# Performance work log

Measured on AMD Instinct MI355X. Metric: run time of the kernel, lower is better.

## Reference

```python
import jax, jax.numpy as jnp
import numpy as np

B, T, E, H = 2, 1024, 1024, 16
D = E // H  # per-head dim = 64; softmax scale uses sqrt(D) per SelfAttentionHead.embedding_dim
SCALE = float(np.sqrt(D))


def setup_inputs() -> dict:
    key = jax.random.key(0)
    ks = jax.random.split(key, 10)
    s = 1.0 / np.sqrt(D)
    sf = 1.0 / np.sqrt(E)
    return {
        "x": jax.random.normal(ks[0], (B, T, E), dtype=jnp.float32),
        # per-head linear params, stacked over head index i: (H, D, D) / (H, D)
        "Wq": jax.random.uniform(ks[1], (H, D, D), minval=-s, maxval=s, dtype=jnp.float32),
        "bq": jax.random.uniform(ks[2], (H, D), minval=-s, maxval=s, dtype=jnp.float32),
        "Wk": jax.random.uniform(ks[3], (H, D, D), minval=-s, maxval=s, dtype=jnp.float32),
        "bk": jax.random.uniform(ks[4], (H, D), minval=-s, maxval=s, dtype=jnp.float32),
        "Wv": jax.random.uniform(ks[5], (H, D, D), minval=-s, maxval=s, dtype=jnp.float32),
        "bv": jax.random.uniform(ks[6], (H, D), minval=-s, maxval=s, dtype=jnp.float32),
        "Wf": jax.random.uniform(ks[7], (E, E), minval=-sf, maxval=sf, dtype=jnp.float32),
        "bf": jax.random.uniform(ks[8], (E,), minval=-sf, maxval=sf, dtype=jnp.float32),
    }


def reference(x, Wq, bq, Wk, bk, Wv, bv, Wf, bf):
    # (B, T, E) -> (B, H, T, D)
    xh = x.reshape(B, T, H, D).transpose(0, 2, 1, 3)
    # each head i applies its own D->D linears to the FULL (B,H,T,D) tensor
    # q/k/v: (B, H, T, I, D) where I indexes the head (param set)
    q = jnp.einsum('bhtd,ied->bhtie', xh, Wq) + bq
    k = jnp.einsum('bhtd,ied->bhtie', xh, Wk) + bk
    v = jnp.einsum('bhtd,ied->bhtie', xh, Wv) + bv
    # attention over the FEATURE dimension: scores are (B,H,I,D,D)
    scores = jnp.einsum('bhtip,bhtiq->bhipq', q, k) / SCALE
    w = jax.nn.softmax(scores, axis=-1)
    # (B,H,I,D,D) x (B,H,T,I,D) -> (B,H,T,I,D)
    o = jnp.einsum('bhipq,bhtiq->bhtip', w, v)
    # concat head outputs along last dim: (B,H,T,I*D) = (B,H,T,E)
    cat = o.reshape(B, H, T, E)
    # final Linear(E,E)
    return jnp.einsum('bhte,fe->bhtf', cat, Wf) + bf
```

## Files before the change

kernel.cpp:

```cpp
#include <hip/hip_runtime.h>

#define TT 1024
#define EE 1024

typedef __attribute__((ext_vector_type(8))) short short8;
typedef __attribute__((ext_vector_type(4))) float floatx4;
typedef __attribute__((ext_vector_type(4))) unsigned short ushort4v;
typedef __attribute__((ext_vector_type(8))) unsigned short ushort8v;

static __device__ __forceinline__ unsigned short f2bf(float f) {
  union { float f; unsigned int u; } v; v.f = f;
  unsigned int u = v.u;
  u += 0x7FFFu + ((u >> 16) & 1u);
  return (unsigned short)(u >> 16);
}
static __device__ __forceinline__ float bf2f(unsigned short u) {
  union { unsigned int i; float f; } v; v.i = ((unsigned int)u) << 16;
  return v.f;
}
static __device__ __forceinline__ void splitbf(float x, unsigned short& h,
                                               unsigned short& l) {
  h = f2bf(x);
  l = f2bf(x - bf2f(h));
}
static __device__ __forceinline__ unsigned short* lp(const unsigned short* t,
                                                     int row, int byte) {
  return (unsigned short*)((const char*)t + row * 128 + (byte ^ ((row & 7) << 4)));
}
static __device__ __forceinline__ short8 ldf(const unsigned short* t, int row,
                                             int byte) {
  return *(const short8*)((const char*)t + row * 128 + (byte ^ ((row & 7) << 4)));
}

__global__ __launch_bounds__(256) void kP(const float* __restrict__ x,
                                          const float* __restrict__ Wf,
                                          float* __restrict__ Sxx_part,
                                          float* __restrict__ sx_part,
                                          unsigned short* __restrict__ Wfbf,
                                          unsigned short* __restrict__ xbf) {
  const int bx = blockIdx.x;
  const int r = threadIdx.x;
  if (bx >= 256) {
    const int wb = bx - 256;
#pragma unroll
    for (int it = 0; it < 4; ++it) {
      int idx = wb * 4096 + it * 1024 + r * 4;
      float4 v = *reinterpret_cast<const float4*>(&Wf[idx]);
      ushort4v o;
      o[0] = f2bf(v.x); o[1] = f2bf(v.y); o[2] = f2bf(v.z); o[3] = f2bf(v.w);
      *reinterpret_cast<ushort4v*>(&Wfbf[idx]) = o;
    }
    return;
  }
  const int bh = bx >> 3, chunk = bx & 7;
  const int b = bh >> 4, h = bh & 15;
  const int t0 = chunk * 128;
  __shared__ float Xs[128 * 64];
  const float* xb = x + ((size_t)b * TT + t0) * EE + h * 64;
#pragma unroll
  for (int j = 0; j < 8; ++j) {
    int idx4 = j * 256 + r;
    int t = idx4 >> 4, c4 = idx4 & 15;
    *reinterpret_cast<float4*>(&Xs[t * 64 + c4 * 4]) =
        *reinterpret_cast<const float4*>(&xb[(size_t)t * EE + c4 * 4]);
  }
  __syncthreads();
#pragma unroll
  for (int j = 0; j < 4; ++j) {
    int idx8 = j * 256 + r;
    int t = idx8 >> 3, gch = idx8 & 7;
    ushort8v o;
#pragma unroll
    for (int e = 0; e < 8; ++e) o[e] = f2bf(Xs[t * 64 + gch * 8 + e]);
    *reinterpret_cast<ushort8v*>(&xbf[((size_t)bh * TT + t0 + t) * 64 + gch * 8]) = o;
  }
  const int p0 = (r >> 4) * 4, q0 = (r & 15) * 4;
  float acc[4][4] = {};
  for (int t = 0; t < 128; ++t) {
    float4 pv = *reinterpret_cast<const float4*>(&Xs[t * 64 + p0]);
    float4 qv = *reinterpret_cast<const float4*>(&Xs[t * 64 + q0]);
    float pa[4] = {pv.x, pv.y, pv.z, pv.w};
    float qa[4] = {qv.x, qv.y, qv.z, qv.w};
#pragma unroll
    for (int i = 0; i < 4; ++i)
#pragma unroll
      for (int j = 0; j < 4; ++j) acc[i][j] += pa[i] * qa[j];
  }
  float* Sb = Sxx_part + ((size_t)chunk * 32 + bh) * 4096;
#pragma unroll
  for (int i = 0; i < 4; ++i) {
    float4 v = make_float4(acc[i][0], acc[i][1], acc[i][2], acc[i][3]);
    *reinterpret_cast<float4*>(&Sb[(p0 + i) * 64 + q0]) = v;
  }
  if (r < 64) {
    float s = 0.f;
    for (int t = 0; t < 128; ++t) s += Xs[t * 64 + r];
    sx_part[(chunk * 32 + bh) * 64 + r] = s;
  }
}

__global__ __launch_bounds__(256) void kB1(const float* __restrict__ Sxx_part,
                                           const float* __restrict__ sx_part,
                                           const float* __restrict__ Wq,
                                           const float* __restrict__ bq,
                                           const float* __restrict__ Wk,
                                           const float* __restrict__ bk,
                                           const float* __restrict__ Wv,
                                           const float* __restrict__ bv,
                                           unsigned short* __restrict__ Mtbf) {
  const int blk = blockIdx.x;
  const int bh = blk >> 4, ih = blk & 15;
  const int r = threadIdx.x;
  const int w = r >> 6, l = r & 63;
  const int wm = w >> 1, wn = w & 1;
  const int lm = l & 15, lk = l >> 4;

  __shared__ unsigned short TSh[4096], TSl[4096];
  __shared__ unsigned short TWh[4096], TWl[4096];
  __shared__ unsigned short TAh[4096], TAl[4096];
  __shared__ float SC[64 * 68];
  __shared__ float svec[64], qsv[64], ksv[64], bqv[64], bkv[64], bvv[64];

#pragma unroll
  for (int it = 0; it < 4; ++it) {
    int idx = it * 1024 + r * 4;
    int row = idx >> 6, c0 = idx & 63;
    float4 vs = *(const float4*)&Sxx_part[(size_t)bh * 4096 + idx];
#pragma unroll
    for (int ch = 1; ch < 8; ++ch) {
      float4 tv = *(const float4*)&Sxx_part[((size_t)ch * 32 + bh) * 4096 + idx];
      vs.x += tv.x; vs.y += tv.y; vs.z += tv.z; vs.w += tv.w;
    }
    float4 vw = *(const float4*)&Wq[ih * 4096 + idx];
    float fs[4] = {vs.x, vs.y, vs.z, vs.w};
    float fw[4] = {vw.x, vw.y, vw.z, vw.w};
    ushort4v sh, sl, wh, wl;
#pragma unroll
    for (int j = 0; j < 4; ++j) {
      unsigned short th, tl;
      splitbf(fs[j], th, tl);
      sh[j] = th; sl[j] = tl;
      splitbf(fw[j], th, tl);
      wh[j] = th; wl[j] = tl;
    }
    *(ushort4v*)lp(TSh, row, c0 * 2) = sh;
    *(ushort4v*)lp(TSl, row, c0 * 2) = sl;
    *(ushort4v*)lp(TWh, row, c0 * 2) = wh;
    *(ushort4v*)lp(TWl, row, c0 * 2) = wl;
  }
  if (r < 64) {
    float s = 0.f;
#pragma unroll
    for (int ch = 0; ch < 8; ++ch) s += sx_part[(ch * 32 + bh) * 64 + r];
    svec[r] = s;
    bqv[r] = bq[ih * 64 + r];
    bkv[r] = bk[ih * 64 + r];
    bvv[r] = bv[ih * 64 + r];
  }
  __syncthreads();

  floatx4 a1[2][2] = {};
  {
    short8 Ah[2][2], Al[2][2], Bh[2][2], Bl[2][2];
#pragma unroll
    for (int mt = 0; mt < 2; ++mt)
#pragma unroll
      for (int ks = 0; ks < 2; ++ks) {
        Ah[mt][ks] = ldf(TWh, wm * 32 + mt * 16 + lm, ks * 64 + lk * 16);
        Al[mt][ks] = ldf(TWl, wm * 32 + mt * 16 + lm, ks * 64 + lk * 16);
        Bh[mt][ks] = ldf(TSh, wn * 32 + mt * 16 + lm, ks * 64 + lk * 16);
        Bl[mt][ks] = ldf(TSl, wn * 32 + mt * 16 + lm, ks * 64 + lk * 16);
      }
#pragma unroll
    for (int ks = 0; ks < 2; ++ks)
#pragma unroll
      for (int mt = 0; mt < 2; ++mt)
#pragma unroll
        for (int nt = 0; nt < 2; ++nt) {
          a1[mt][nt] = __builtin_amdgcn_mfma_f32_16x16x32_bf16(Ah[mt][ks], Bh[nt][ks], a1[mt][nt], 0, 0, 0);
          a1[mt][nt] = __builtin_amdgcn_mfma_f32_16x16x32_bf16(Ah[mt][ks], Bl[nt][ks], a1[mt][nt], 0, 0, 0);
          a1[mt][nt] = __builtin_amdgcn_mfma_f32_16x16x32_bf16(Al[mt][ks], Bh[nt][ks], a1[mt][nt], 0, 0, 0);
        }
  }
#pragma unroll
  for (int mt = 0; mt < 2; ++mt)
#pragma unroll
    for (int nt = 0; nt < 2; ++nt)
#pragma unroll
      for (int q = 0; q < 4; ++q) {
        int p = wm * 32 + mt * 16 + lk * 4 + q;
        int dd = wn * 32 + nt * 16 + lm;
        unsigned short h, lo2;
        splitbf(a1[mt][nt][q], h, lo2);
        *lp(TAh, p, dd * 2) = h;
        *lp(TAl, p, dd * 2) = lo2;
      }
  {
    int p = r >> 2, dc = (r & 3) * 16;
    float s = 0.f;
#pragma unroll
    for (int j = 0; j < 16; ++j) {
      int d = dc + j;
      s += (bf2f(*lp(TWh, p, d * 2)) + bf2f(*lp(TWl, p, d * 2))) * svec[d];
    }
    s += __shfl_xor(s, 1);
    s += __shfl_xor(s, 2);
    if ((r & 3) == 0) qsv[p] = s;
  }
  __syncthreads();

#pragma unroll
  for (int it = 0; it < 4; ++it) {
    int idx = it * 1024 + r * 4;
    int row = idx >> 6, c0 = idx & 63;
    float4 vw = *(const float4*)&Wk[ih * 4096 + idx];
    float fw[4] = {vw.x, vw.y, vw.z, vw.w};
    ushort4v wh, wl;
#pragma unroll
    for (int j = 0; j < 4; ++j) {
      unsigned short th, tl;
      splitbf(fw[j], th, tl);
      wh[j] = th; wl[j] = tl;
    }
    *(ushort4v*)lp(TWh, row, c0 * 2) = wh;
    *(ushort4v*)lp(TWl, row, c0 * 2) = wl;
    float4 vv = *(const float4*)&Wv[ih * 4096 + idx];
    int q = row, d0 = c0;
    *lp(TSh, d0 + 0, q * 2) = f2bf(vv.x);
    *lp(TSh, d0 + 1, q * 2) = f2bf(vv.y);
    *lp(TSh, d0 + 2, q * 2) = f2bf(vv.z);
    *lp(TSh, d0 + 3, q * 2) = f2bf(vv.w);
  }
  __syncthreads();
  {
    int p = r >> 2, dc = (r & 3) * 16;
    float s = 0.f;
#pragma unroll
    for (int j = 0; j < 16; ++j) {
      int d = dc + j;
      s += (bf2f(*lp(TWh, p, d * 2)) + bf2f(*lp(TWl, p, d * 2))) * svec[d];
    }
    s += __shfl_xor(s, 1);
    s += __shfl_xor(s, 2);
    if ((r & 3) == 0) ksv[p] = s;
  }
  floatx4 a2[2][2] = {};
  {
    short8 Ah[2][2], Al[2][2], Bh[2][2], Bl[2][2];
#pragma unroll
    for (int mt = 0; mt < 2; ++mt)
#pragma unroll
      for (int ks = 0; ks < 2; ++ks) {
        Ah[mt][ks] = ldf(TAh, wm * 32 + mt * 16 + lm, ks * 64 + lk * 16);
        Al[mt][ks] = ldf(TAl, wm * 32 + mt * 16 + lm, ks * 64 + lk * 16);
        Bh[mt][ks] = ldf(TWh, wn * 32 + mt * 16 + lm, ks * 64 + lk * 16);
        Bl[mt][ks] = ldf(TWl, wn * 32 + mt * 16 + lm, ks * 64 + lk * 16);
      }
#pragma unroll
    for (int ks = 0; ks < 2; ++ks)
#pragma unroll
      for (int mt = 0; mt < 2; ++mt)
#pragma unroll
        for (int nt = 0; nt < 2; ++nt) {
          a2[mt][nt] = __builtin_amdgcn_mfma_f32_16x16x32_bf16(Ah[mt][ks], Bh[nt][ks], a2[mt][nt], 0, 0, 0);
          a2[mt][nt] = __builtin_amdgcn_mfma_f32_16x16x32_bf16(Ah[mt][ks], Bl[nt][ks], a2[mt][nt], 0, 0, 0);
          a2[mt][nt] = __builtin_amdgcn_mfma_f32_16x16x32_bf16(Al[mt][ks], Bh[nt][ks], a2[mt][nt], 0, 0, 0);
        }
  }
  __syncthreads();
#pragma unroll
  for (int mt = 0; mt < 2; ++mt)
#pragma unroll
    for (int nt = 0; nt < 2; ++nt)
#pragma unroll
      for (int q = 0; q < 4; ++q) {
        int p = wm * 32 + mt * 16 + lk * 4 + q;
        int qq = wn * 32 + nt * 16 + lm;
        float v = a2[mt][nt][q] + qsv[p] * bkv[qq] + bqv[p] * ksv[qq] +
                  1024.f * bqv[p] * bkv[qq];
        SC[p * 68 + qq] = v * 0.125f;
      }
  __syncthreads();
  {
    int p = r >> 2, qc = (r & 3) * 16;
    float e[16];
    float m = -1e30f;
#pragma unroll
    for (int j = 0; j < 16; ++j) {
      e[j] = SC[p * 68 + qc + j];
      m = fmaxf(m, e[j]);
    }
    m = fmaxf(m, __shfl_xor(m, 1));
    m = fmaxf(m, __shfl_xor(m, 2));
    float s = 0.f, cp = 0.f;
#pragma unroll
    for (int j = 0; j < 16; ++j) {
      float ex = __expf(e[j] - m);
      e[j] = ex;
      s += ex;
      cp += ex * bvv[qc + j];
    }
    s += __shfl_xor(s, 1);
    s += __shfl_xor(s, 2);
    cp += __shfl_xor(cp, 1);
    cp += __shfl_xor(cp, 2);
    float inv = 1.f / s;
#pragma unroll
    for (int j = 0; j < 16; ++j) *lp(TSl, p, (qc + j) * 2) = f2bf(e[j] * inv);
    if ((r & 3) == 0)
      Mtbf[(size_t)(2048 + bh) * 1024 + ih * 64 + p] = f2bf(cp * inv);
  }
  __syncthreads();
  floatx4 a3[2][2] = {};
  {
    short8 A3[2][2], B3[2][2];
#pragma unroll
    for (int mt = 0; mt < 2; ++mt)
#pragma unroll
      for (int ks = 0; ks < 2; ++ks) {
        A3[mt][ks] = ldf(TSh, wm * 32 + mt * 16 + lm, ks * 64 + lk * 16);
        B3[mt][ks] = ldf(TSl, wn * 32 + mt * 16 + lm, ks * 64 + lk * 16);
      }
#pragma unroll
    for (int ks = 0; ks < 2; ++ks)
#pragma unroll
      for (int mt = 0; mt < 2; ++mt)
#pragma unroll
        for (int nt = 0; nt < 2; ++nt)
          a3[mt][nt] = __builtin_amdgcn_mfma_f32_16x16x32_bf16(A3[mt][ks], B3[nt][ks], a3[mt][nt], 0, 0, 0);
  }
#pragma unroll
  for (int mt = 0; mt < 2; ++mt)
#pragma unroll
    for (int nt = 0; nt < 2; ++nt)
#pragma unroll
      for (int q = 0; q < 4; ++q) {
        int d = wm * 32 + mt * 16 + lk * 4 + q;
        int p = wn * 32 + nt * 16 + lm;
        Mtbf[(size_t)(bh * 64 + d) * 1024 + ih * 64 + p] = f2bf(a3[mt][nt][q]);
      }
}

__global__ __launch_bounds__(256) void kC(const unsigned short* __restrict__ xbf,
                                          const unsigned short* __restrict__ Wfbf,
                                          const unsigned short* __restrict__ Mtbf,
                                          const float* __restrict__ bfv,
                                          float* __restrict__ out) {
  const int fx = blockIdx.x, bh = blockIdx.y;
  const int f0 = fx * 128;
  const int r = threadIdx.x;
  const int w = r >> 6, l = r & 63;
  const int lm = l & 15, lk = l >> 4;

  __shared__ __align__(16) unsigned short GT[128 * 64];
  __shared__ __align__(16) unsigned short cL[1024];
  __shared__ float gL[128];

  if (r < 128)
    *reinterpret_cast<ushort8v*>(&cL[r * 8]) = *reinterpret_cast<const ushort8v*>(
        &Mtbf[(size_t)(2048 + bh) * 1024 + r * 8]);
  __syncthreads();

  {
    const int wf = w >> 1, wd = w & 1;
    const unsigned short* ap = Wfbf + (size_t)(f0 + wf * 64 + lm) * 1024 + lk * 8;
    const unsigned short* bp = Mtbf + (size_t)(bh * 64 + wd * 32 + lm) * 1024 + lk * 8;
    floatx4 acc[4][2] = {};
    floatx4 gacc[4] = {};
    for (int k0 = 0; k0 < 1024; k0 += 64) {
      short8 a[4][2], b[2][2], cf[2];
#pragma unroll
      for (int mi = 0; mi < 4; ++mi)
#pragma unroll
        for (int ks = 0; ks < 2; ++ks)
          a[mi][ks] = *reinterpret_cast<const short8*>(ap + mi * 16 * 1024 + k0 + ks * 32);
#pragma unroll
      for (int ni = 0; ni < 2; ++ni)
#pragma unroll
        for (int ks = 0; ks < 2; ++ks)
          b[ni][ks] = *reinterpret_cast<const short8*>(bp + ni * 16 * 1024 + k0 + ks * 32);
#pragma unroll
      for (int ks = 0; ks < 2; ++ks)
        cf[ks] = *reinterpret_cast<const short8*>(&cL[k0 + ks * 32 + lk * 8]);
#pragma unroll
      for (int ks = 0; ks < 2; ++ks)
#pragma unroll
        for (int mi = 0; mi < 4; ++mi) {
#pragma unroll
          for (int ni = 0; ni < 2; ++ni)
            acc[mi][ni] = __builtin_amdgcn_mfma_f32_16x16x32_bf16(
                a[mi][ks], b[ni][ks], acc[mi][ni], 0, 0, 0);
          if (wd == 0)
            gacc[mi] = __builtin_amdgcn_mfma_f32_16x16x32_bf16(
                a[mi][ks], cf[ks], gacc[mi], 0, 0, 0);
        }
    }
#pragma unroll
    for (int mi = 0; mi < 4; ++mi)
#pragma unroll
      for (int ni = 0; ni < 2; ++ni)
#pragma unroll
        for (int q = 0; q < 4; ++q) {
          int fl = wf * 64 + mi * 16 + lk * 4 + q;
          int d = wd * 32 + ni * 16 + lm;
          *lp(GT, fl, d * 2) = f2bf(acc[mi][ni][q]);
        }
    if (wd == 0 && lm == 0) {
#pragma unroll
      for (int mi = 0; mi < 4; ++mi)
#pragma unroll
        for (int q = 0; q < 4; ++q) {
          int fl = wf * 64 + mi * 16 + lk * 4 + q;
          gL[fl] = gacc[mi][q] + bfv[f0 + fl];
        }
    }
  }
  __syncthreads();

  const int wt = w >> 1, wc = w & 1;
  float gv[4];
#pragma unroll
  for (int ni = 0; ni < 4; ++ni) gv[ni] = gL[wc * 64 + ni * 16 + lm];
  short8 bfr[4][2];
#pragma unroll
  for (int ni = 0; ni < 4; ++ni)
#pragma unroll
    for (int ks = 0; ks < 2; ++ks)
      bfr[ni][ks] = ldf(GT, wc * 64 + ni * 16 + lm, (ks * 32 + lk * 8) * 2);
  float* ob = out + (size_t)bh * 1048576;
  for (int t0 = 0; t0 < 1024; t0 += 128) {
    const unsigned short* ap =
        xbf + (size_t)bh * 65536 + (size_t)(t0 + wt * 64 + lm) * 64 + lk * 8;
    short8 a[4][2];
#pragma unroll
    for (int mi = 0; mi < 4; ++mi)
#pragma unroll
      for (int ks = 0; ks < 2; ++ks)
        a[mi][ks] = *reinterpret_cast<const short8*>(ap + mi * 16 * 64 + ks * 32);
    floatx4 acc[4][4] = {};
#pragma unroll
    for (int ks = 0; ks < 2; ++ks)
#pragma unroll
      for (int mi = 0; mi < 4; ++mi)
#pragma unroll
        for (int ni = 0; ni < 4; ++ni)
          acc[mi][ni] = __builtin_amdgcn_mfma_f32_16x16x32_bf16(
              a[mi][ks], bfr[ni][ks], acc[mi][ni], 0, 0, 0);
#pragma unroll
    for (int mi = 0; mi < 4; ++mi)
#pragma unroll
      for (int ni = 0; ni < 4; ++ni) {
        const int f = f0 + wc * 64 + ni * 16 + lm;
#pragma unroll
        for (int q = 0; q < 4; ++q) {
          const int t = t0 + wt * 64 + mi * 16 + lk * 4 + q;
          ob[(size_t)t * 1024 + f] = acc[mi][ni][q] + gv[ni];
        }
      }
  }
}

extern "C" void kernel_launch(void* const* d_in, const int* in_sizes, int n_in,
                              void* d_out, int out_size, void* d_ws, size_t ws_size,
                              hipStream_t stream) {
  const float* x = (const float*)d_in[0];
  const float* Wq = (const float*)d_in[1];
  const float* bq = (const float*)d_in[2];
  const float* Wk = (const float*)d_in[3];
  const float* bk = (const float*)d_in[4];
  const float* Wv = (const float*)d_in[5];
  const float* bv = (const float*)d_in[6];
  const float* Wf = (const float*)d_in[7];
  const float* bf = (const float*)d_in[8];
  float* out = (float*)d_out;

  float* ws = (float*)d_ws;
  float* Sxx_part = ws;
  float* sx_part = Sxx_part + 1048576;
  unsigned short* Wfbf = (unsigned short*)(sx_part + 16384);
  unsigned short* xbf = Wfbf + 1048576;
  unsigned short* Mtbf = xbf + 2097152;

  kP<<<512, 256, 0, stream>>>(x, Wf, Sxx_part, sx_part, Wfbf, xbf);
  kB1<<<512, 256, 0, stream>>>(Sxx_part, sx_part, Wq, bq, Wk, bk, Wv, bv, Mtbf);
  kC<<<dim3(8, 32), 256, 0, stream>>>(xbf, Wfbf, Mtbf, bf, out);
}
```

Measured before the change: 82.25 us.

## Rebalance kernel grids, alias kB1 shared memory, vectorize kC output stores

kP now gives each block 256 time steps in two 128-row passes, which halves the number of partial Gram matrices kB1 has to reduce. kB1 lets the W/A staging tiles share storage with the score buffer, cutting its LDS footprint so more blocks can fit per CU. kC uses 64-wide feature tiles, doubling its grid to 512 blocks, and swaps the MFMA operand roles so each lane writes a float4 of contiguous features instead of scattered scalar stores. The cost is that kC reads the Mtbf/Wf GEMM operands twice as often, and kP runs fewer blocks, each with more serial work.

```diff
diff --git a/kernel.cpp b/kernel.cpp
--- a/kernel.cpp
+++ b/kernel.cpp
@@ -40,8 +40,8 @@
                                           unsigned short* __restrict__ xbf) {
   const int bx = blockIdx.x;
   const int r = threadIdx.x;
-  if (bx >= 256) {
-    const int wb = bx - 256;
+  if (bx >= 128) {
+    const int wb = bx - 128;
 #pragma unroll
     for (int it = 0; it < 4; ++it) {
       int idx = wb * 4096 + it * 1024 + r * 4;
@@ -52,39 +52,47 @@
     }
     return;
   }
-  const int bh = bx >> 3, chunk = bx & 7;
+  const int bh = bx >> 2, chunk = bx & 3;
   const int b = bh >> 4, h = bh & 15;
-  const int t0 = chunk * 128;
   __shared__ float Xs[128 * 64];
-  const float* xb = x + ((size_t)b * TT + t0) * EE + h * 64;
-#pragma unroll
-  for (int j = 0; j < 8; ++j) {
-    int idx4 = j * 256 + r;
-    int t = idx4 >> 4, c4 = idx4 & 15;
-    *reinterpret_cast<float4*>(&Xs[t * 64 + c4 * 4]) =
-        *reinterpret_cast<const float4*>(&xb[(size_t)t * EE + c4 * 4]);
-  }
-  __syncthreads();
-#pragma unroll
-  for (int j = 0; j < 4; ++j) {
-    int idx8 = j * 256 + r;
-    int t = idx8 >> 3, gch = idx8 & 7;
-    ushort8v o;
-#pragma unroll
-    for (int e = 0; e < 8; ++e) o[e] = f2bf(Xs[t * 64 + gch * 8 + e]);
-    *reinterpret_cast<ushort8v*>(&xbf[((size_t)bh * TT + t0 + t) * 64 + gch * 8]) = o;
-  }
   const int p0 = (r >> 4) * 4, q0 = (r & 15) * 4;
   float acc[4][4] = {};
-  for (int t = 0; t < 128; ++t) {
-    float4 pv = *reinterpret_cast<const float4*>(&Xs[t * 64 + p0]);
-    float4 qv = *reinterpret_cast<const float4*>(&Xs[t * 64 + q0]);
-    float pa[4] = {pv.x, pv.y, pv.z, pv.w};
-    float qa[4] = {qv.x, qv.y, qv.z, qv.w};
-#pragma unroll
-    for (int i = 0; i < 4; ++i)
-#pragma unroll
-      for (int j = 0; j < 4; ++j) acc[i][j] += pa[i] * qa[j];
+  float sxa = 0.f;
+#pragma unroll
+  for (int half = 0; half < 2; ++half) {
+    const int t0 = chunk * 256 + half * 128;
+    const float* xb = x + ((size_t)b * TT + t0) * EE + h * 64;
+#pragma unroll
+    for (int j = 0; j < 8; ++j) {
+      int idx4 = j * 256 + r;
+      int t = idx4 >> 4, c4 = idx4 & 15;
+      *reinterpret_cast<float4*>(&Xs[t * 64 + c4 * 4]) =
+          *reinterpret_cast<const float4*>(&xb[(size_t)t * EE + c4 * 4]);
+    }
+    __syncthreads();
+#pragma unroll
+    for (int j = 0; j < 4; ++j) {
+      int idx8 = j * 256 + r;
+      int t = idx8 >> 3, gch = idx8 & 7;
+      ushort8v o;
+#pragma unroll
+      for (int e = 0; e < 8; ++e) o[e] = f2bf(Xs[t * 64 + gch * 8 + e]);
+      *reinterpret_cast<ushort8v*>(&xbf[((size_t)bh * TT + t0 + t) * 64 + gch * 8]) = o;
+    }
+    for (int t = 0; t < 128; ++t) {
+      float4 pv = *reinterpret_cast<const float4*>(&Xs[t * 64 + p0]);
+      float4 qv = *reinterpret_cast<const float4*>(&Xs[t * 64 + q0]);
+      float pa[4] = {pv.x, pv.y, pv.z, pv.w};
+      float qa[4] = {qv.x, qv.y, qv.z, qv.w};
+#pragma unroll
+      for (int i = 0; i < 4; ++i)
+#pragma unroll
+        for (int j = 0; j < 4; ++j) acc[i][j] += pa[i] * qa[j];
+    }
+    if (r < 64) {
+      for (int t = 0; t < 128; ++t) sxa += Xs[t * 64 + r];
+    }
+    __syncthreads();
   }
   float* Sb = Sxx_part + ((size_t)chunk * 32 + bh) * 4096;
 #pragma unroll
@@ -92,11 +100,7 @@
     float4 v = make_float4(acc[i][0], acc[i][1], acc[i][2], acc[i][3]);
     *reinterpret_cast<float4*>(&Sb[(p0 + i) * 64 + q0]) = v;
   }
-  if (r < 64) {
-    float s = 0.f;
-    for (int t = 0; t < 128; ++t) s += Xs[t * 64 + r];
-    sx_part[(chunk * 32 + bh) * 64 + r] = s;
-  }
+  if (r < 64) sx_part[(chunk * 32 + bh) * 64 + r] = sxa;
 }
 
 __global__ __launch_bounds__(256) void kB1(const float* __restrict__ Sxx_part,
@@ -115,11 +119,16 @@
   const int wm = w >> 1, wn = w & 1;
   const int lm = l & 15, lk = l >> 4;
 
-  __shared__ unsigned short TSh[4096], TSl[4096];
-  __shared__ unsigned short TWh[4096], TWl[4096];
-  __shared__ unsigned short TAh[4096], TAl[4096];
-  __shared__ float SC[64 * 68];
-  __shared__ float svec[64], qsv[64], ksv[64], bqv[64], bkv[64], bvv[64];
+  __shared__ __align__(16) unsigned short TSh[4096], TSl[4096];
+  __shared__ __align__(16) unsigned short TBig[16384];
+  __shared__ float sf[384];
+  float* svec = sf;       float* qsv = sf + 64;  float* ksv = sf + 128;
+  float* bqv = sf + 192;  float* bkv = sf + 256; float* bvv = sf + 320;
+  unsigned short* TWh = TBig;
+  unsigned short* TWl = TBig + 4096;
+  unsigned short* TAh = TBig + 8192;
+  unsigned short* TAl = TBig + 12288;
+  float* SC = (float*)TBig;
 
 #pragma unroll
   for (int it = 0; it < 4; ++it) {
@@ -127,7 +136,7 @@
     int row = idx >> 6, c0 = idx & 63;
     float4 vs = *(const float4*)&Sxx_part[(size_t)bh * 4096 + idx];
 #pragma unroll
-    for (int ch = 1; ch < 8; ++ch) {
+    for (int ch = 1; ch < 4; ++ch) {
       float4 tv = *(const float4*)&Sxx_part[((size_t)ch * 32 + bh) * 4096 + idx];
       vs.x += tv.x; vs.y += tv.y; vs.z += tv.z; vs.w += tv.w;
     }
@@ -151,7 +160,7 @@
   if (r < 64) {
     float s = 0.f;
 #pragma unroll
-    for (int ch = 0; ch < 8; ++ch) s += sx_part[(ch * 32 + bh) * 64 + r];
+    for (int ch = 0; ch < 4; ++ch) s += sx_part[(ch * 32 + bh) * 64 + r];
     svec[r] = s;
     bqv[r] = bq[ih * 64 + r];
     bkv[r] = bk[ih * 64 + r];
@@ -347,14 +356,15 @@
                                           const float* __restrict__ bfv,
                                           float* __restrict__ out) {
   const int fx = blockIdx.x, bh = blockIdx.y;
-  const int f0 = fx * 128;
+  const int f0 = fx * 64;
   const int r = threadIdx.x;
   const int w = r >> 6, l = r & 63;
   const int lm = l & 15, lk = l >> 4;
-
-  __shared__ __align__(16) unsigned short GT[128 * 64];
+  const int wa = w >> 1, wb = w & 1;
+
+  __shared__ __align__(16) unsigned short GT[64 * 64];
   __shared__ __align__(16) unsigned short cL[1024];
-  __shared__ float gL[128];
+  __shared__ float gL[64];
 
   if (r < 128)
     *reinterpret_cast<ushort8v*>(&cL[r * 8]) = *reinterpret_cast<const ushort8v*>(
@@ -362,15 +372,14 @@
   __syncthreads();
 
   {
-    const int wf = w >> 1, wd = w & 1;
-    const unsigned short* ap = Wfbf + (size_t)(f0 + wf * 64 + lm) * 1024 + lk * 8;
-    const unsigned short* bp = Mtbf + (size_t)(bh * 64 + wd * 32 + lm) * 1024 + lk * 8;
-    floatx4 acc[4][2] = {};
-    floatx4 gacc[4] = {};
+    const unsigned short* ap = Wfbf + (size_t)(f0 + wa * 32 + lm) * 1024 + lk * 8;
+    const unsigned short* bp = Mtbf + (size_t)(bh * 64 + wb * 32 + lm) * 1024 + lk * 8;
+    floatx4 acc[2][2] = {};
+    floatx4 gacc[2] = {};
     for (int k0 = 0; k0 < 1024; k0 += 64) {
-      short8 a[4][2], b[2][2], cf[2];
-#pragma unroll
-      for (int mi = 0; mi < 4; ++mi)
+      short8 a[2][2], b[2][2], cf[2];
+#pragma unroll
+      for (int mi = 0; mi < 2; ++mi)
 #pragma unroll
         for (int ks = 0; ks < 2; ++ks)
           a[mi][ks] = *reinterpret_cast<const short8*>(ap + mi * 16 * 1024 + k0 + ks * 32);
@@ -385,78 +394,78 @@
 #pragma unroll
       for (int ks = 0; ks < 2; ++ks)
 #pragma unroll
-        for (int mi = 0; mi < 4; ++mi) {
+        for (int mi = 0; mi < 2; ++mi) {
 #pragma unroll
           for (int ni = 0; ni < 2; ++ni)
             acc[mi][ni] = __builtin_amdgcn_mfma_f32_16x16x32_bf16(
                 a[mi][ks], b[ni][ks], acc[mi][ni], 0, 0, 0);
-          if (wd == 0)
+          if (wb == 0)
             gacc[mi] = __builtin_amdgcn_mfma_f32_16x16x32_bf16(
                 a[mi][ks], cf[ks], gacc[mi], 0, 0, 0);
         }
     }
 #pragma unroll
-    for (int mi = 0; mi < 4; ++mi)
+    for (int mi = 0; mi < 2; ++mi)
 #pragma unroll
       for (int ni = 0; ni < 2; ++ni)
 #pragma unroll
         for (int q = 0; q < 4; ++q) {
-          int fl = wf * 64 + mi * 16 + lk * 4 + q;
-          int d = wd * 32 + ni * 16 + lm;
+          int fl = wa * 32 + mi * 16 + lk * 4 + q;
+          int d = wb * 32 + ni * 16 + lm;
           *lp(GT, fl, d * 2) = f2bf(acc[mi][ni][q]);
         }
-    if (wd == 0 && lm == 0) {
-#pragma unroll
-      for (int mi = 0; mi < 4; ++mi)
+    if (wb == 0 && lm == 0) {
+#pragma unroll
+      for (int mi = 0; mi < 2; ++mi)
 #pragma unroll
         for (int q = 0; q < 4; ++q) {
-          int fl = wf * 64 + mi * 16 + lk * 4 + q;
+          int fl = wa * 32 + mi * 16 + lk * 4 + q;
           gL[fl] = gacc[mi][q] + bfv[f0 + fl];
         }
     }
   }
   __syncthreads();
 
-  const int wt = w >> 1, wc = w & 1;
-  float gv[4];
-#pragma unroll
-  for (int ni = 0; ni < 4; ++ni) gv[ni] = gL[wc * 64 + ni * 16 + lm];
-  short8 bfr[4][2];
-#pragma unroll
-  for (int ni = 0; ni < 4; ++ni)
+  short8 afr[2][2];
+#pragma unroll
+  for (int mi = 0; mi < 2; ++mi)
 #pragma unroll
     for (int ks = 0; ks < 2; ++ks)
-      bfr[ni][ks] = ldf(GT, wc * 64 + ni * 16 + lm, (ks * 32 + lk * 8) * 2);
+      afr[mi][ks] = ldf(GT, wa * 32 + mi * 16 + lm, ks * 64 + lk * 16);
+  float4 gv[2];
+#pragma unroll
+  for (int mi = 0; mi < 2; ++mi)
+    gv[mi] = *reinterpret_cast<const float4*>(&gL[wa * 32 + mi * 16 + lk * 4]);
   float* ob = out + (size_t)bh * 1048576;
   for (int t0 = 0; t0 < 1024; t0 += 128) {
-    const unsigned short* ap =
-        xbf + (size_t)bh * 65536 + (size_t)(t0 + wt * 64 + lm) * 64 + lk * 8;
-    short8 a[4][2];
-#pragma unroll
-    for (int mi = 0; mi < 4; ++mi)
+    const unsigned short* bp =
+        xbf + (size_t)bh * 65536 + (size_t)(t0 + wb * 64 + lm) * 64 + lk * 8;
+    short8 b[4][2];
+#pragma unroll
+    for (int ni = 0; ni < 4; ++ni)
 #pragma unroll
       for (int ks = 0; ks < 2; ++ks)
-        a[mi][ks] = *reinterpret_cast<const short8*>(ap + mi * 16 * 64 + ks * 32);
-    floatx4 acc[4][4] = {};
+        b[ni][ks] = *reinterpret_cast<const short8*>(bp + ni * 16 * 64 + ks * 32);
+    floatx4 acc[2][4] = {};
 #pragma unroll
     for (int ks = 0; ks < 2; ++ks)
 #pragma unroll
-      for (int mi = 0; mi < 4; ++mi)
+      for (int mi = 0; mi < 2; ++mi)
 #pragma unroll
         for (int ni = 0; ni < 4; ++ni)
           acc[mi][ni] = __builtin_amdgcn_mfma_f32_16x16x32_bf16(
-              a[mi][ks], bfr[ni][ks], acc[mi][ni], 0, 0, 0);
-#pragma unroll
-    for (int mi = 0; mi < 4; ++mi)
+              afr[mi][ks], b[ni][ks], acc[mi][ni], 0, 0, 0);
+#pragma unroll
+    for (int mi = 0; mi < 2; ++mi) {
+      const int f = f0 + wa * 32 + mi * 16 + lk * 4;
 #pragma unroll
       for (int ni = 0; ni < 4; ++ni) {
-        const int f = f0 + wc * 64 + ni * 16 + lm;
-#pragma unroll
-        for (int q = 0; q < 4; ++q) {
-          const int t = t0 + wt * 64 + mi * 16 + lk * 4 + q;
-          ob[(size_t)t * 1024 + f] = acc[mi][ni][q] + gv[ni];
-        }
-      }
+        const int t = t0 + wb * 64 + ni * 16 + lm;
+        float4 o = make_float4(acc[mi][ni][0] + gv[mi].x, acc[mi][ni][1] + gv[mi].y,
+                               acc[mi][ni][2] + gv[mi].z, acc[mi][ni][3] + gv[mi].w);
+        *reinterpret_cast<float4*>(&ob[(size_t)t * 1024 + f]) = o;
+      }
+    }
   }
 }
 
@@ -476,12 +485,12 @@
 
   float* ws = (float*)d_ws;
   float* Sxx_part = ws;
-  float* sx_part = Sxx_part + 1048576;
-  unsigned short* Wfbf = (unsigned short*)(sx_part + 16384);
+  float* sx_part = Sxx_part + 524288;
+  unsigned short* Wfbf = (unsigned short*)(sx_part + 8192);
   unsigned short* xbf = Wfbf + 1048576;
   unsigned short* Mtbf = xbf + 2097152;
 
-  kP<<<512, 256, 0, stream>>>(x, Wf, Sxx_part, sx_part, Wfbf, xbf);
+  kP<<<384, 256, 0, stream>>>(x, Wf, Sxx_part, sx_part, Wfbf, xbf);
   kB1<<<512, 256, 0, stream>>>(Sxx_part, sx_part, Wq, bq, Wk, bk, Wv, bv, Mtbf);
-  kC<<<dim3(8, 32), 256, 0, stream>>>(xbf, Wfbf, Mtbf, bf, out);
-}
+  kC<<<dim3(16, 32), 256, 0, stream>>>(xbf, Wfbf, Mtbf, bf, out);
+}
```

Measured after the change: 93.91 us. 14.2% more time.
